# Kernel optimization log

Hardware: AMD Instinct MI355X
Metric: run time of the kernel (lower is better)

The kernel has to match this reference:

```python
import jax, jax.numpy as jnp
import numpy as np

WIRES = 4

def _ry(theta):
    # theta: scalar or (N,) -> (2,2) or (N,2,2) complex64
    c = jnp.cos(theta / 2)
    s = jnp.sin(theta / 2)
    return jnp.stack([jnp.stack([c, -s], -1), jnp.stack([s, c], -1)], -2).astype(jnp.complex64)

def _rz(phi):
    e = jnp.exp(-0.5j * phi.astype(jnp.complex64))
    z = jnp.zeros_like(e)
    return jnp.stack([jnp.stack([e, z], -1), jnp.stack([z, jnp.conj(e)], -1)], -2)

def _apply(state, U, w):
    # state: (N,2,2,2,2); wire w lives on axis 1+w
    state = jnp.moveaxis(state, 1 + w, -1)
    if U.ndim == 2:
        state = jnp.einsum('ij,n...j->n...i', U, state)
    else:
        state = jnp.einsum('nij,n...j->n...i', U, state)
    return jnp.moveaxis(state, -1, 1 + w)

def _cnot(state, c, t):
    # flip target axis where control axis == 1
    s0, s1 = jnp.split(state, 2, axis=1 + c)
    s1 = jnp.flip(s1, axis=1 + t)
    return jnp.concatenate([s0, s1], axis=1 + c)

def _quanv(patches, q_params):
    # patches: (N,4) angles; q_params: (L,4,3). Batched 4-qubit statevector sim.
    N = patches.shape[0]
    state = jnp.zeros((N, 16), jnp.complex64).at[:, 0].set(1.0).reshape(N, 2, 2, 2, 2)
    num_layers = q_params.shape[0]
    for i in range(num_layers):
        for w in range(WIRES):
            state = _apply(state, _ry(patches[:, w]), w)
        for w in range(WIRES):
            state = _cnot(state, w, (w + 1) % WIRES)
        for w in range(WIRES):
            state = _apply(state, _rz(q_params[i, w, 0]), w)
            state = _apply(state, _ry(q_params[i, w, 1]), w)
            state = _apply(state, _rz(q_params[i, w, 2]), w)
    probs = jnp.abs(state) ** 2  # (N,2,2,2,2)
    zsign = jnp.array([1.0, -1.0], jnp.float32)
    ez = [jnp.sum(probs * zsign.reshape((1,) + (1,) * w + (2,) + (1,) * (WIRES - 1 - w)),
                  axis=(1, 2, 3, 4)) for w in range(WIRES)]
    return jnp.stack(ez, -1)  # (N,4) <Z_j> expectations

def setup_inputs() -> dict:
    key = jax.random.key(0)
    k1, k2, k3 = jax.random.split(key, 3)
    B = 1024
    x = jax.random.normal(k1, (B, 1, 28, 28), dtype=jnp.float32)
    q_params = jax.random.normal(k2, (3, 4, 3), dtype=jnp.float32)
    W = jax.random.normal(k3, (10, 784), dtype=jnp.float32) * 0.03
    b = jnp.zeros((10,), jnp.float32)
    return {"x": x, "q_params": q_params, "W": W, "b": b}

def reference(x, q_params, W, b):
    B = x.shape[0]
    # extract 2x2 patches in (row-block, col-block) order, each flattened row-major
    patches = x.reshape(B, 14, 2, 14, 2).transpose(0, 1, 3, 2, 4).reshape(B * 196, 4)
    feats = _quanv(patches, q_params).reshape(B, 196 * 4)  # cat order: patch-major, 4 wires each
    logits = feats @ W.T + b
    return jax.nn.log_softmax(logits, axis=-1)
```

## Files before the change

kernel.cpp:

```cpp
#include <hip/hip_runtime.h>
#include <math.h>


#define APPLY_RY(ST, cc, ss) do { \
  _Pragma("unroll") \
  for (int i = 0; i < 16; ++i) { \
    if (!(i & (ST))) { \
      float ar = sr[i], ai = si[i], br = sr[i + (ST)], bi = si[i + (ST)]; \
      sr[i]        = (cc) * ar - (ss) * br; \
      si[i]        = (cc) * ai - (ss) * bi; \
      sr[i + (ST)] = (ss) * ar + (cc) * br; \
      si[i + (ST)] = (ss) * ai + (cc) * bi; \
    } } } while (0)

#define APPLY_CNOT(SC, ST) do { \
  _Pragma("unroll") \
  for (int i = 0; i < 16; ++i) { \
    if ((i & (SC)) && !(i & (ST))) { \
      float tr = sr[i], ti = si[i]; \
      sr[i] = sr[i + (ST)]; si[i] = si[i + (ST)]; \
      sr[i + (ST)] = tr;    si[i + (ST)] = ti; \
    } } } while (0)

#define APPLY_U(ST, U0R, U0I, U1R, U1I) do { \
  _Pragma("unroll") \
  for (int i = 0; i < 16; ++i) { \
    if (!(i & (ST))) { \
      float ar = sr[i], ai = si[i], br = sr[i + (ST)], bi = si[i + (ST)]; \
      sr[i]        =  (U0R) * ar - (U0I) * ai + (U1R) * br - (U1I) * bi; \
      si[i]        =  (U0R) * ai + (U0I) * ar + (U1R) * bi + (U1I) * br; \
      sr[i + (ST)] = -(U1R) * ar - (U1I) * ai + (U0R) * br + (U0I) * bi; \
      si[i + (ST)] = -(U1R) * ai + (U1I) * ar + (U0R) * bi - (U0I) * br; \
    } } } while (0)

#define APPLY_U_LDS(ST, l, w) do { \
  const float* u_ = &uu[((l) * 4 + (w)) * 4]; \
  float u0r = u_[0], u0i = u_[1], u1r = u_[2], u1i = u_[3]; \
  APPLY_U(ST, u0r, u0i, u1r, u1i); \
} while (0)

#define LAYER_TAIL(l) do { \
  APPLY_CNOT(8, 4); APPLY_CNOT(4, 2); APPLY_CNOT(2, 1); APPLY_CNOT(1, 8); \
  APPLY_U_LDS(8, l, 0); APPLY_U_LDS(4, l, 1); APPLY_U_LDS(2, l, 2); APPLY_U_LDS(1, l, 3); \
} while (0)

#define DATA_RY_ALL() do { \
  APPLY_RY(8, dc[0], ds[0]); APPLY_RY(4, dc[1], ds[1]); \
  APPLY_RY(2, dc[2], ds[2]); APPLY_RY(1, dc[3], ds[3]); \
} while (0)

template <int LC>
__global__ __launch_bounds__(256, 4) void quanv_fused_kernel(
    const float* __restrict__ x,
    const float* __restrict__ qp,
    const float* __restrict__ W,
    const float* __restrict__ bias,
    float* __restrict__ out,
    int Lrt)
{
  const int L = (LC > 0) ? LC : Lrt;
  const int n   = blockIdx.x;
  const int tid = threadIdx.x;
  const int p   = tid;

  __shared__ float uu[8 * 16];
  if (tid < 4 * L) {
    const int l = tid >> 2, w = tid & 3;
    const float p0 = qp[l * 12 + w * 3 + 0];
    const float p1 = qp[l * 12 + w * 3 + 1];
    const float p2 = qp[l * 12 + w * 3 + 2];
    float c, s, ca, sa, cb, sb;
    __sincosf(0.5f * p1, &s, &c);
    __sincosf(0.5f * (p0 + p2), &sa, &ca);
    __sincosf(0.5f * (p0 - p2), &sb, &cb);
    float* u_ = &uu[(l * 4 + w) * 4];
    u_[0] =  c * ca;
    u_[1] = -c * sa;
    u_[2] = -s * cb;
    u_[3] = -s * sb;
  }
  __syncthreads();

  float ez[4] = {0.f, 0.f, 0.f, 0.f};

  if (p < 196) {
    const int pr = p / 14, pcc = p % 14;
    const float2* xb = (const float2*)(x + (size_t)n * 784 + (2 * pr) * 28 + 2 * pcc);
    float2 top = xb[0], bot = xb[14];
    float dc[4], ds[4];
    __sincosf(0.5f * top.x, &ds[0], &dc[0]);
    __sincosf(0.5f * top.y, &ds[1], &dc[1]);
    __sincosf(0.5f * bot.x, &ds[2], &dc[2]);
    __sincosf(0.5f * bot.y, &ds[3], &dc[3]);

    float sr[16], si[16];

    if (LC > 0) {
      float p00 = dc[0] * dc[1], p01 = dc[0] * ds[1];
      float p10 = ds[0] * dc[1], p11 = ds[0] * ds[1];
      float q00 = dc[2] * dc[3], q01 = dc[2] * ds[3];
      float q10 = ds[2] * dc[3], q11 = ds[2] * ds[3];
      float hi[4] = {p00, p01, p10, p11};
      float lo[4] = {q00, q01, q10, q11};
#pragma unroll
      for (int i = 0; i < 16; ++i) { sr[i] = hi[i >> 2] * lo[i & 3]; si[i] = 0.f; }
      LAYER_TAIL(0);
#pragma unroll
      for (int l = 1; l < ((LC > 0) ? LC : 1); ++l) {
        DATA_RY_ALL();
        LAYER_TAIL(l);
      }
    } else {
#pragma unroll
      for (int i = 0; i < 16; ++i) { sr[i] = 0.f; si[i] = 0.f; }
      sr[0] = 1.f;
      for (int l = 0; l < L; ++l) {
        DATA_RY_ALL();
        LAYER_TAIL(l);
      }
    }

#pragma unroll
    for (int i = 0; i < 16; ++i) {
      float pp = sr[i] * sr[i] + si[i] * si[i];
      ez[0] += (i & 8) ? -pp : pp;
      ez[1] += (i & 4) ? -pp : pp;
      ez[2] += (i & 2) ? -pp : pp;
      ez[3] += (i & 1) ? -pp : pp;
    }
  }

  float part[10];
#pragma unroll
  for (int c = 0; c < 10; ++c) part[c] = 0.f;
  if (p < 196) {
    const float4* Wv = (const float4*)W;
#pragma unroll
    for (int c = 0; c < 10; ++c) {
      float4 wc = Wv[c * 196 + p];
      part[c] = ez[0] * wc.x + ez[1] * wc.y + ez[2] * wc.z + ez[3] * wc.w;
    }
  }

  const int lane = tid & 63;
  const int wave = tid >> 6;
  __shared__ float red[4][10];
#pragma unroll
  for (int c = 0; c < 10; ++c) {
    float v = part[c];
#pragma unroll
    for (int off = 32; off > 0; off >>= 1) v += __shfl_down(v, off, 64);
    if (lane == 0) red[wave][c] = v;
  }
  __syncthreads();

  if (tid == 0) {
    float logits[10];
    float m = -1e30f;
#pragma unroll
    for (int c = 0; c < 10; ++c) {
      logits[c] = red[0][c] + red[1][c] + red[2][c] + red[3][c] + bias[c];
      m = fmaxf(m, logits[c]);
    }
    float sum = 0.f;
#pragma unroll
    for (int c = 0; c < 10; ++c) sum += __expf(logits[c] - m);
    float lse = m + __logf(sum);
#pragma unroll
    for (int c = 0; c < 10; ++c) out[(size_t)n * 10 + c] = logits[c] - lse;
  }
}

extern "C" void kernel_launch(void* const* d_in, const int* in_sizes, int n_in,
                              void* d_out, int out_size, void* d_ws, size_t ws_size,
                              hipStream_t stream) {
  const float* x    = (const float*)d_in[0];
  const float* qp   = (const float*)d_in[1];
  const float* W    = (const float*)d_in[2];
  const float* bias = (const float*)d_in[3];
  float* out        = (float*)d_out;

  const int B = in_sizes[0] / 784;
  const int L = in_sizes[1] / 12;

  switch (L) {
    case 1: quanv_fused_kernel<1><<<B, 256, 0, stream>>>(x, qp, W, bias, out, L); break;
    case 2: quanv_fused_kernel<2><<<B, 256, 0, stream>>>(x, qp, W, bias, out, L); break;
    case 3: quanv_fused_kernel<3><<<B, 256, 0, stream>>>(x, qp, W, bias, out, L); break;
    case 4: quanv_fused_kernel<4><<<B, 256, 0, stream>>>(x, qp, W, bias, out, L); break;
    default: quanv_fused_kernel<0><<<B, 256, 0, stream>>>(x, qp, W, bias, out, L); break;
  }
}
```

Measured before the change: 81.99 us.

## Fold data RY into trainable unitary and compute final layer analytically in Z-measurement

Merges each layer's data-dependent RY gate with the following trainable single-qubit unitary into one combined 2x2 gate per wire, so one gate pass runs where two did. The last layer's single-qubit unitaries are not applied to the state at all. Their effect on each <Z> expectation is folded into precomputed Bloch-rotation coefficients combined with reduced-density-matrix terms of the state after the final CNOT ring. This cuts per-thread gate arithmetic at the cost of a few extra reduction terms and some added algebraic complexity.

After: 92.31 us. +12.6%, slower.

```diff
diff --git a/kernel.cpp b/kernel.cpp
--- a/kernel.cpp
+++ b/kernel.cpp
@@ -1,26 +1,6 @@
 #include <hip/hip_runtime.h>
 #include <math.h>
 
-
-#define APPLY_RY(ST, cc, ss) do { \
-  _Pragma("unroll") \
-  for (int i = 0; i < 16; ++i) { \
-    if (!(i & (ST))) { \
-      float ar = sr[i], ai = si[i], br = sr[i + (ST)], bi = si[i + (ST)]; \
-      sr[i]        = (cc) * ar - (ss) * br; \
-      si[i]        = (cc) * ai - (ss) * bi; \
-      sr[i + (ST)] = (ss) * ar + (cc) * br; \
-      si[i + (ST)] = (ss) * ai + (cc) * bi; \
-    } } } while (0)
-
-#define APPLY_CNOT(SC, ST) do { \
-  _Pragma("unroll") \
-  for (int i = 0; i < 16; ++i) { \
-    if ((i & (SC)) && !(i & (ST))) { \
-      float tr = sr[i], ti = si[i]; \
-      sr[i] = sr[i + (ST)]; si[i] = si[i + (ST)]; \
-      sr[i + (ST)] = tr;    si[i + (ST)] = ti; \
-    } } } while (0)
 
 #define APPLY_U(ST, U0R, U0I, U1R, U1I) do { \
   _Pragma("unroll") \
@@ -33,20 +13,27 @@
       si[i + (ST)] = -(U1R) * ai + (U1I) * ar + (U0R) * bi - (U0I) * br; \
     } } } while (0)
 
-#define APPLY_U_LDS(ST, l, w) do { \
+#define APPLY_V(ST, l, w) do { \
   const float* u_ = &uu[((l) * 4 + (w)) * 4]; \
   float u0r = u_[0], u0i = u_[1], u1r = u_[2], u1i = u_[3]; \
-  APPLY_U(ST, u0r, u0i, u1r, u1i); \
+  float v0r = dc[w] * u0r + ds[w] * u1r; \
+  float v0i = dc[w] * u0i - ds[w] * u1i; \
+  float v1r = dc[w] * u1r - ds[w] * u0r; \
+  float v1i = dc[w] * u1i + ds[w] * u0i; \
+  APPLY_U(ST, v0r, v0i, v1r, v1i); \
 } while (0)
 
-#define LAYER_TAIL(l) do { \
+#define APPLY_CNOT(SC, ST) do { \
+  _Pragma("unroll") \
+  for (int i = 0; i < 16; ++i) { \
+    if ((i & (SC)) && !(i & (ST))) { \
+      float tr = sr[i], ti = si[i]; \
+      sr[i] = sr[i + (ST)]; si[i] = si[i + (ST)]; \
+      sr[i + (ST)] = tr;    si[i + (ST)] = ti; \
+    } } } while (0)
+
+#define CNOT_RING() do { \
   APPLY_CNOT(8, 4); APPLY_CNOT(4, 2); APPLY_CNOT(2, 1); APPLY_CNOT(1, 8); \
-  APPLY_U_LDS(8, l, 0); APPLY_U_LDS(4, l, 1); APPLY_U_LDS(2, l, 2); APPLY_U_LDS(1, l, 3); \
-} while (0)
-
-#define DATA_RY_ALL() do { \
-  APPLY_RY(8, dc[0], ds[0]); APPLY_RY(4, dc[1], ds[1]); \
-  APPLY_RY(2, dc[2], ds[2]); APPLY_RY(1, dc[3], ds[3]); \
 } while (0)
 
 template <int LC>
@@ -64,6 +51,7 @@
   const int p   = tid;
 
   __shared__ float uu[8 * 16];
+  __shared__ float mm[4][3];
   if (tid < 4 * L) {
     const int l = tid >> 2, w = tid & 3;
     const float p0 = qp[l * 12 + w * 3 + 0];
@@ -73,11 +61,16 @@
     __sincosf(0.5f * p1, &s, &c);
     __sincosf(0.5f * (p0 + p2), &sa, &ca);
     __sincosf(0.5f * (p0 - p2), &sb, &cb);
-    float* u_ = &uu[(l * 4 + w) * 4];
-    u_[0] =  c * ca;
-    u_[1] = -c * sa;
-    u_[2] = -s * cb;
-    u_[3] = -s * sb;
+    const float u0r =  c * ca, u0i = -c * sa;
+    const float u1r = -s * cb, u1i = -s * sb;
+    if (l == L - 1) {
+      mm[w][0] = (u0r * u0r + u0i * u0i) - (u1r * u1r + u1i * u1i);
+      mm[w][1] = 4.0f * (u0r * u1r + u0i * u1i);
+      mm[w][2] = 4.0f * (u0r * u1i - u0i * u1r);
+    } else {
+      float* u_ = &uu[(l * 4 + w) * 4];
+      u_[0] = u0r; u_[1] = u0i; u_[2] = u1r; u_[3] = u1i;
+    }
   }
   __syncthreads();
 
@@ -95,38 +88,43 @@
 
     float sr[16], si[16];
 
-    if (LC > 0) {
-      float p00 = dc[0] * dc[1], p01 = dc[0] * ds[1];
-      float p10 = ds[0] * dc[1], p11 = ds[0] * ds[1];
-      float q00 = dc[2] * dc[3], q01 = dc[2] * ds[3];
-      float q10 = ds[2] * dc[3], q11 = ds[2] * ds[3];
-      float hi[4] = {p00, p01, p10, p11};
-      float lo[4] = {q00, q01, q10, q11};
+    {
+      float hi[4] = {dc[0] * dc[1], dc[0] * ds[1], ds[0] * dc[1], ds[0] * ds[1]};
+      float lo[4] = {dc[2] * dc[3], dc[2] * ds[3], ds[2] * dc[3], ds[2] * ds[3]};
 #pragma unroll
       for (int i = 0; i < 16; ++i) { sr[i] = hi[i >> 2] * lo[i & 3]; si[i] = 0.f; }
-      LAYER_TAIL(0);
+    }
+    CNOT_RING();
+
+    if (LC > 0) {
 #pragma unroll
-      for (int l = 1; l < ((LC > 0) ? LC : 1); ++l) {
-        DATA_RY_ALL();
-        LAYER_TAIL(l);
+      for (int l = 0; l < ((LC > 0) ? LC - 1 : 0); ++l) {
+        APPLY_V(8, l, 0); APPLY_V(4, l, 1); APPLY_V(2, l, 2); APPLY_V(1, l, 3);
+        CNOT_RING();
       }
     } else {
-#pragma unroll
-      for (int i = 0; i < 16; ++i) { sr[i] = 0.f; si[i] = 0.f; }
-      sr[0] = 1.f;
-      for (int l = 0; l < L; ++l) {
-        DATA_RY_ALL();
-        LAYER_TAIL(l);
+      for (int l = 0; l < L - 1; ++l) {
+        APPLY_V(8, l, 0); APPLY_V(4, l, 1); APPLY_V(2, l, 2); APPLY_V(1, l, 3);
+        CNOT_RING();
       }
     }
 
+    float pp[16];
 #pragma unroll
-    for (int i = 0; i < 16; ++i) {
-      float pp = sr[i] * sr[i] + si[i] * si[i];
-      ez[0] += (i & 8) ? -pp : pp;
-      ez[1] += (i & 4) ? -pp : pp;
-      ez[2] += (i & 2) ? -pp : pp;
-      ez[3] += (i & 1) ? -pp : pp;
+    for (int i = 0; i < 16; ++i) pp[i] = sr[i] * sr[i] + si[i] * si[i];
+#pragma unroll
+    for (int w = 0; w < 4; ++w) {
+      const int st = 8 >> w;
+      float zs = 0.f, re = 0.f, im = 0.f;
+#pragma unroll
+      for (int i = 0; i < 16; ++i) {
+        if (!(i & st)) {
+          zs += pp[i] - pp[i + st];
+          re += sr[i] * sr[i + st] + si[i] * si[i + st];
+          im += sr[i] * si[i + st] - si[i] * sr[i + st];
+        }
+      }
+      ez[w] = mm[w][0] * zs + mm[w][1] * re - mm[w][2] * im;
     }
   }
 
```
